# Kernel tuning notes

Hardware: AMD Instinct MI355X
Metric: run time of the kernel (lower is better)

## Reference

```python
import jax, jax.numpy as jnp
import numpy as np

B, I, HID, H, KS = 64, 1024, 2048, 8, 4
D = HID // H  # head_size = 256; also BlockDiagonal block size = (2*I)//H = 256
EPS = 1e-5


def setup_inputs() -> dict:
    key = jax.random.key(0)
    ks = jax.random.split(key, 16)
    r = lambda i, shape, s=0.02: jax.random.normal(ks[i], shape, dtype=jnp.float32) * s
    z = lambda shape: jnp.zeros(shape, jnp.float32)
    return {
        "x": jax.random.normal(ks[0], (B, I), dtype=jnp.float32),
        "h_prev": z((B, H, D)),
        "c_prev": z((B, H, D, D)),
        "n_prev": z((B, H, D)),
        "m_prev": z((B, H)),
        "ln_w": jnp.ones((I,), jnp.float32), "ln_b": z((I,)),
        "W_ul": r(1, (I, HID)), "b_ul": z((HID,)),
        "W_ur": r(2, (I, HID)), "b_ur": z((HID,)),
        "W_conv": r(3, (HID, HID, KS)), "b_conv": z((HID,)),
        "W_skip": r(4, (HID, HID)), "b_skip": z((HID,)),
        "W_q": r(5, (H, D, D)), "b_q": z((HID,)),
        "W_k": r(6, (H, D, D)), "b_k": z((HID,)),
        "W_v": r(7, (H, D, D)), "b_v": z((HID,)),
        "W_i": r(8, (HID, H)), "b_i": z((H,)),
        "W_f": r(9, (HID, H)), "b_f": z((H,)),
        "W_o": r(10, (HID, HID)), "b_o": z((HID,)),
        "W_down": r(11, (HID, I)), "b_down": z((I,)),
        "gn_w": jnp.ones((HID,), jnp.float32), "gn_b": z((HID,)),
    }


def _block_diag(zf, W, b):
    # BlockDiagonal: chunk last dim into H blocks, per-block Linear, concat -> [B,H,D]
    zh = zf.reshape(zf.shape[0], H, -1)
    return jnp.einsum('bhi,hio->bho', zh, W) + b.reshape(H, -1)


def reference(x, h_prev, c_prev, n_prev, m_prev, ln_w, ln_b, W_ul, b_ul, W_ur, b_ur,
              W_conv, b_conv, W_skip, b_skip, W_q, b_q, W_k, b_k, W_v, b_v,
              W_i, b_i, W_f, b_f, W_o, b_o, W_down, b_down, gn_w, gn_b):
    # LayerNorm
    mu = x.mean(-1, keepdims=True)
    var = jnp.mean((x - mu) ** 2, -1, keepdims=True)
    xn = (x - mu) * jax.lax.rsqrt(var + EPS) * ln_w + ln_b
    # Up projections
    xl = xn @ W_ul + b_ul            # [B, 2I] == [B, HID]
    xr = xn @ W_ur + b_ur
    # Causal conv over a length-1 sequence: after left padding + slicing, only the
    # last kernel tap (index KS-1) touches real data -> linear map with W_conv[:,:,KS-1]
    xc = jax.nn.silu(xl @ W_conv[:, :, KS - 1].T + b_conv)
    x_skip = xc @ W_skip + b_skip    # [B, HID]
    q = _block_diag(xc, W_q, b_q)                       # [B,H,D]
    k = _block_diag(xc, W_k, b_k) / jnp.sqrt(jnp.float32(D))
    v = _block_diag(xl, W_v, b_v)
    i_t = xc @ W_i + b_i             # [B,H]
    f_t = xc @ W_f + b_f
    o = jax.nn.sigmoid(xl @ W_o + b_o).reshape(-1, H, D)
    # Stabilized exponential gating
    m_t = jnp.maximum(f_t + m_prev, i_t)
    i_g = jnp.exp(i_t - m_t)
    f_g = jnp.exp(f_t + m_prev - m_t)
    # Outer-product state update + bilinear readout
    c_t = f_g[..., None, None] * c_prev + i_g[..., None, None] * jnp.einsum('bhd,bhk->bhdk', v, k)
    n_t = f_g[..., None] * n_prev + i_g[..., None] * k
    num = jnp.einsum('bhdk,bhk->bhd', c_t, q)
    den = jnp.clip(jnp.einsum('bhd,bhd->bh', n_t, q), 1.0, None)[..., None]
    h_t = o * num / den              # [B,H,D]
    # GroupNorm with num_groups == num_heads: normalize per head
    g_mu = h_t.mean(-1, keepdims=True)
    g_var = jnp.mean((h_t - g_mu) ** 2, -1, keepdims=True)
    gn = ((h_t - g_mu) * jax.lax.rsqrt(g_var + EPS)).reshape(-1, HID) * gn_w + gn_b
    out = (gn + x_skip) * jax.nn.silu(xr)
    out = out @ W_down + b_down
    final = out + x
    return (final, h_t, c_t, n_t, m_t)
```

## Files before the change

### kernel.cpp

```cpp
#include <hip/hip_runtime.h>
#include <cstddef>

typedef __bf16 bf16;
typedef __bf16 bf16x8 __attribute__((ext_vector_type(8)));
typedef short  s16x8  __attribute__((ext_vector_type(8)));
typedef float  f32x4  __attribute__((ext_vector_type(4)));

template <class T> T&& declv() noexcept;
template <class, class = void> struct takes_bf16vec { static constexpr bool value = false; };
template <class V> struct takes_bf16vec<V, decltype((void)__builtin_amdgcn_mfma_f32_16x16x32_bf16(
    declv<V>(), declv<V>(), declv<f32x4>(), 0, 0, 0))> { static constexpr bool value = true; };

template <class V>
__device__ __forceinline__ f32x4 mfma_bf16_16x16x32(V a, V b, f32x4 c) {
  if constexpr (takes_bf16vec<V>::value) {
    return __builtin_amdgcn_mfma_f32_16x16x32_bf16(a, b, c, 0, 0, 0);
  } else {
    return __builtin_amdgcn_mfma_f32_16x16x32_bf16(
        __builtin_bit_cast(s16x8, a), __builtin_bit_cast(s16x8, b), c, 0, 0, 0);
  }
}

constexpr int M_NONE = 0, M_SILU = 1, M_SIG = 2;

__global__ __launch_bounds__(256) void repack_wc(const float* __restrict__ Wc,
                                                 bf16* __restrict__ Wp) {
  const int n = blockIdx.x;
  const float4* src = (const float4*)(Wc + (size_t)n * 8192);
  bf16* dst = Wp + (size_t)n * 2048;
  for (int k = threadIdx.x; k < 2048; k += 256) {
    const float4 t = src[k];
    dst[k] = (bf16)t.w;
  }
}

__global__ __launch_bounds__(256) void ln_kernel(const float* __restrict__ x,
                                                 const float* __restrict__ w,
                                                 const float* __restrict__ bs,
                                                 const float* __restrict__ bdown,
                                                 bf16* __restrict__ xn,
                                                 float* __restrict__ outf) {
  const int b = blockIdx.x, tid = threadIdx.x;
  __shared__ float red[256];
  float vals[4];
  float s = 0.f;
#pragma unroll
  for (int i = 0; i < 4; ++i) { vals[i] = x[b * 1024 + i * 256 + tid]; s += vals[i]; }
  red[tid] = s; __syncthreads();
  for (int off = 128; off; off >>= 1) { if (tid < off) red[tid] += red[tid + off]; __syncthreads(); }
  const float mu = red[0] * (1.f / 1024.f);
  __syncthreads();
  float s2 = 0.f;
#pragma unroll
  for (int i = 0; i < 4; ++i) { const float d = vals[i] - mu; s2 += d * d; }
  red[tid] = s2; __syncthreads();
  for (int off = 128; off; off >>= 1) { if (tid < off) red[tid] += red[tid + off]; __syncthreads(); }
  const float rs = rsqrtf(red[0] * (1.f / 1024.f) + 1e-5f);
#pragma unroll
  for (int i = 0; i < 4; ++i) {
    const int j = i * 256 + tid;
    xn[b * 1024 + j] = (bf16)((vals[i] - mu) * rs * w[j] + bs[j]);
    outf[b * 1024 + j] = vals[i] + bdown[j];
  }
}

template <int K, int KS, int NTILES, bool BT, bool DUAL, bool ATOMIC>
__global__ __launch_bounds__(256) void gemm_part(
    const bf16* __restrict__ A0, const bf16* __restrict__ A1,
    const float* __restrict__ W0, const float* __restrict__ W1,
    const bf16* __restrict__ Wb,
    int ldA, int ldB, float* __restrict__ dst, int outN) {
  constexpr int Ncomb = NTILES * 16;
  constexpr int Kslice = K / KS;
  constexpr int chunk = Kslice / 4;
  const int tid = threadIdx.x;
  const int lane = tid & 63, wave = tid >> 6;
  const int l15 = lane & 15, quad = lane >> 4;
  const int tile = blockIdx.x % NTILES, ks = blockIdx.x / NTILES;

  const bf16* A = A0;
  const float* W = W0;
  int ncol;
  if (DUAL) {
    const int seg = tile >> 7;
    if (seg) { A = A1; W = W1; }
    ncol = (tile & 127) * 16;
  } else {
    ncol = tile * 16;
  }
  const int kbeg = ks * Kslice + wave * chunk;

  f32x4 acc0{}, acc1{}, acc2{}, acc3{};
#pragma unroll
  for (int k = 0; k < chunk; k += 32) {
    const int kk = kbeg + k + quad * 8;
    bf16x8 bfrag;
    if (BT) {
      bfrag = *(const bf16x8*)(Wb + (size_t)(ncol + l15) * K + kk);
    } else {
      const float* wp = W + (size_t)kk * ldB + ncol + l15;
#pragma unroll
      for (int j = 0; j < 8; ++j) bfrag[j] = (bf16)wp[(size_t)j * ldB];
    }
    const bf16* ap = A + (size_t)l15 * ldA + kk;
    const size_t st = (size_t)16 * ldA;
    bf16x8 a0 = *(const bf16x8*)(ap);
    bf16x8 a1 = *(const bf16x8*)(ap + st);
    bf16x8 a2 = *(const bf16x8*)(ap + 2 * st);
    bf16x8 a3 = *(const bf16x8*)(ap + 3 * st);
    acc0 = mfma_bf16_16x16x32(a0, bfrag, acc0);
    acc1 = mfma_bf16_16x16x32(a1, bfrag, acc1);
    acc2 = mfma_bf16_16x16x32(a2, bfrag, acc2);
    acc3 = mfma_bf16_16x16x32(a3, bfrag, acc3);
  }
  __shared__ float lds[4][64][20];
#pragma unroll
  for (int r = 0; r < 4; ++r) {
    const int rr = quad * 4 + r;
    lds[wave][rr][l15]      = acc0[r];
    lds[wave][16 + rr][l15] = acc1[r];
    lds[wave][32 + rr][l15] = acc2[r];
    lds[wave][48 + rr][l15] = acc3[r];
  }
  __syncthreads();
  const int col = tid & 15, rb = (tid >> 4) << 2;
#pragma unroll
  for (int r2 = 0; r2 < 4; ++r2) {
    const int row = rb + r2;
    const float v = lds[0][row][col] + lds[1][row][col] + lds[2][row][col] + lds[3][row][col];
    if (ATOMIC) {
      atomicAdd(dst + (size_t)row * outN + tile * 16 + col, v);
    } else {
      dst[((size_t)ks * 64 + row) * Ncomb + tile * 16 + col] = v;
    }
  }
}

__global__ __launch_bounds__(256) void combine(
    const float* __restrict__ part, int KS, int Ncomb, int halfN,
    const float* __restrict__ bias0, const float* __restrict__ bias1,
    int mode0, int mode1,
    float* __restrict__ outF0, bf16* __restrict__ outB0,
    float* __restrict__ outF1, bf16* __restrict__ outB1) {
  const int e = (blockIdx.x * 256 + threadIdx.x) * 4;
  const int total = 64 * Ncomb;
  if (e >= total) return;
  const int row = e / Ncomb, col = e - row * Ncomb;
  float4 s = *(const float4*)(part + e);
  for (int ks = 1; ks < KS; ++ks) {
    const float4 p = *(const float4*)(part + (size_t)ks * total + e);
    s.x += p.x; s.y += p.y; s.z += p.z; s.w += p.w;
  }
  const int seg = (col >= halfN) ? 1 : 0;
  const int cn = col - seg * halfN;
  const float* bias = seg ? bias1 : bias0;
  const int mode = seg ? mode1 : mode0;
  float* outF = seg ? outF1 : outF0;
  bf16* outB = seg ? outB1 : outB0;
  float vv[4] = {s.x, s.y, s.z, s.w};
#pragma unroll
  for (int j = 0; j < 4; ++j) {
    float v = vv[j] + bias[cn + j];
    if (mode == M_SILU)       v = v / (1.f + expf(-v));
    else if (mode == M_SIG)   v = 1.f / (1.f + expf(-v));
    const size_t oi = (size_t)row * halfN + cn + j;
    if (outF) outF[oi] = v;
    if (outB) outB[oi] = (bf16)v;
  }
}

__global__ __launch_bounds__(256) void gemm_qkv(
    const bf16* __restrict__ xc, const bf16* __restrict__ xl,
    const float* __restrict__ Wq, const float* __restrict__ bq,
    const float* __restrict__ Wk, const float* __restrict__ bk,
    const float* __restrict__ Wv, const float* __restrict__ bv,
    float* __restrict__ qf, float* __restrict__ kf, float* __restrict__ vf) {
  const int tid = threadIdx.x;
  const int lane = tid & 63, wave = tid >> 6;
  const int l15 = lane & 15, quad = lane >> 4;
  const int seg = blockIdx.x >> 7, t = blockIdx.x & 127;
  const int n0 = t * 16, h = t >> 4, wn0 = n0 & 255;
  const bf16* A = (seg == 2) ? xl : xc;
  const float* W = (seg == 0) ? Wq : (seg == 1) ? Wk : Wv;
  const float* bias = (seg == 0) ? bq : (seg == 1) ? bk : bv;
  float* out = (seg == 0) ? qf : (seg == 1) ? kf : vf;
  const float* Wb = W + (size_t)h * 65536;
  const int aCol0 = h << 8;
  const int kbeg = wave * 64;

  f32x4 acc0{}, acc1{}, acc2{}, acc3{};
#pragma unroll
  for (int k = 0; k < 64; k += 32) {
    const int kk = kbeg + k + quad * 8;
    bf16x8 bfrag;
    const float* wp = Wb + (size_t)kk * 256 + wn0 + l15;
#pragma unroll
    for (int j = 0; j < 8; ++j) bfrag[j] = (bf16)wp[(size_t)j * 256];
    const bf16* ap = A + (size_t)l15 * 2048 + aCol0 + kk;
    const size_t st = (size_t)16 * 2048;
    bf16x8 a0 = *(const bf16x8*)(ap);
    bf16x8 a1 = *(const bf16x8*)(ap + st);
    bf16x8 a2 = *(const bf16x8*)(ap + 2 * st);
    bf16x8 a3 = *(const bf16x8*)(ap + 3 * st);
    acc0 = mfma_bf16_16x16x32(a0, bfrag, acc0);
    acc1 = mfma_bf16_16x16x32(a1, bfrag, acc1);
    acc2 = mfma_bf16_16x16x32(a2, bfrag, acc2);
    acc3 = mfma_bf16_16x16x32(a3, bfrag, acc3);
  }
  __shared__ float lds[4][64][20];
#pragma unroll
  for (int r = 0; r < 4; ++r) {
    const int rr = quad * 4 + r;
    lds[wave][rr][l15]      = acc0[r];
    lds[wave][16 + rr][l15] = acc1[r];
    lds[wave][32 + rr][l15] = acc2[r];
    lds[wave][48 + rr][l15] = acc3[r];
  }
  __syncthreads();
  const int col = tid & 15, rb = (tid >> 4) << 2;
  const float bv_ = bias[n0 + col];
#pragma unroll
  for (int r2 = 0; r2 < 4; ++r2) {
    const int row = rb + r2;
    float v = lds[0][row][col] + lds[1][row][col] + lds[2][row][col] + lds[3][row][col] + bv_;
    if (seg == 1) v *= 0.0625f;
    out[(size_t)row * 2048 + n0 + col] = v;
  }
}

__global__ __launch_bounds__(256) void gates_kernel(
    const bf16* __restrict__ xc, const float* __restrict__ Wi, const float* __restrict__ bi,
    const float* __restrict__ Wf, const float* __restrict__ bfv, const float* __restrict__ m_prev,
    float* __restrict__ ig, float* __restrict__ fg, float* __restrict__ mt_out) {
  const int b = blockIdx.x, tid = threadIdx.x;
  float ai[8] = {}, af[8] = {};
  for (int k = tid; k < 2048; k += 256) {
    const float xv = (float)xc[b * 2048 + k];
    const float4 wi0 = *(const float4*)(Wi + (size_t)k * 8);
    const float4 wi1 = *(const float4*)(Wi + (size_t)k * 8 + 4);
    const float4 wf0 = *(const float4*)(Wf + (size_t)k * 8);
    const float4 wf1 = *(const float4*)(Wf + (size_t)k * 8 + 4);
    ai[0] += xv * wi0.x; ai[1] += xv * wi0.y; ai[2] += xv * wi0.z; ai[3] += xv * wi0.w;
    ai[4] += xv * wi1.x; ai[5] += xv * wi1.y; ai[6] += xv * wi1.z; ai[7] += xv * wi1.w;
    af[0] += xv * wf0.x; af[1] += xv * wf0.y; af[2] += xv * wf0.z; af[3] += xv * wf0.w;
    af[4] += xv * wf1.x; af[5] += xv * wf1.y; af[6] += xv * wf1.z; af[7] += xv * wf1.w;
  }
  __shared__ float ri[256][8], rf[256][8];
#pragma unroll
  for (int h = 0; h < 8; ++h) { ri[tid][h] = ai[h]; rf[tid][h] = af[h]; }
  __syncthreads();
  for (int off = 128; off; off >>= 1) {
    if (tid < off) {
#pragma unroll
      for (int h = 0; h < 8; ++h) { ri[tid][h] += ri[tid + off][h]; rf[tid][h] += rf[tid + off][h]; }
    }
    __syncthreads();
  }
  if (tid < 8) {
    const float it = ri[0][tid] + bi[tid];
    const float ft = rf[0][tid] + bfv[tid];
    const float mp = m_prev[b * 8 + tid];
    const float mt = fmaxf(ft + mp, it);
    mt_out[b * 8 + tid] = mt;
    ig[b * 8 + tid] = expf(it - mt);
    fg[b * 8 + tid] = expf(ft + mp - mt);
  }
}

__global__ __launch_bounds__(256) void state1(
    const float* __restrict__ c_prev, const float* __restrict__ qf,
    const float* __restrict__ kf, const float* __restrict__ vf,
    const float* __restrict__ ig, const float* __restrict__ fg,
    float* __restrict__ ct_out, float* __restrict__ numw) {
  const int bh = blockIdx.x >> 3, rg = blockIdx.x & 7;
  const int tid = threadIdx.x;
  const int b = bh >> 3, h = bh & 7, vb = b * 2048 + h * 256;
  __shared__ float q_s[256], k_s[256];
  q_s[tid] = qf[vb + tid];
  k_s[tid] = kf[vb + tid];
  __syncthreads();
  const float i_g = ig[bh], f_g = fg[bh];
  const int row = rg * 32 + (tid >> 3);
  const int lane8 = tid & 7;
  const float vd = vf[vb + row];
  const float iv = i_g * vd;
  const size_t base = ((size_t)bh << 16) + ((size_t)row << 8) + lane8 * 4;
  float p = 0.f;
#pragma unroll
  for (int i = 0; i < 8; ++i) {
    const int c = lane8 * 4 + i * 32;
    const float4 cp = *(const float4*)(c_prev + base + i * 32);
    float4 cn;
    cn.x = f_g * cp.x + iv * k_s[c];
    cn.y = f_g * cp.y + iv * k_s[c + 1];
    cn.z = f_g * cp.z + iv * k_s[c + 2];
    cn.w = f_g * cp.w + iv * k_s[c + 3];
    *(float4*)(ct_out + base + i * 32) = cn;
    p += cn.x * q_s[c] + cn.y * q_s[c + 1] + cn.z * q_s[c + 2] + cn.w * q_s[c + 3];
  }
#pragma unroll
  for (int m = 1; m < 8; m <<= 1) p += __shfl_xor(p, m, 64);
  if (lane8 == 0) numw[bh * 256 + row] = p;
}

__global__ __launch_bounds__(256) void state2(
    const float* __restrict__ n_prev, const float* __restrict__ qf,
    const float* __restrict__ kf, const float* __restrict__ of,
    const float* __restrict__ ig, const float* __restrict__ fg,
    const float* numw, const float* __restrict__ xskip,
    const float* __restrict__ xrf, const float* __restrict__ gnw,
    const float* __restrict__ gnb, float* __restrict__ nt_out,
    float* ht_out, bf16* __restrict__ pre_bf) {
  const int bh = blockIdx.x, b = bh >> 3, h = bh & 7;
  const int tid = threadIdx.x;
  const int vb = b * 2048 + h * 256;
  __shared__ float red[256];
  const float i_g = ig[bh], f_g = fg[bh];
  const float qv = qf[vb + tid], kv = kf[vb + tid];
  const float nv = f_g * n_prev[bh * 256 + tid] + i_g * kv;
  nt_out[bh * 256 + tid] = nv;
  red[tid] = nv * qv;
  __syncthreads();
  for (int off = 128; off; off >>= 1) { if (tid < off) red[tid] += red[tid + off]; __syncthreads(); }
  const float den = fmaxf(red[0], 1.0f);
  const float num = numw[bh * 256 + tid];
  const float hv = of[vb + tid] * num / den;
  ht_out[bh * 256 + tid] = hv;
  __syncthreads();
  red[tid] = hv; __syncthreads();
  for (int off = 128; off; off >>= 1) { if (tid < off) red[tid] += red[tid + off]; __syncthreads(); }
  const float mu = red[0] * (1.f / 256.f);
  __syncthreads();
  const float dv = hv - mu;
  red[tid] = dv * dv; __syncthreads();
  for (int off = 128; off; off >>= 1) { if (tid < off) red[tid] += red[tid + off]; __syncthreads(); }
  const float gn = (hv - mu) * rsqrtf(red[0] * (1.f / 256.f) + 1e-5f);
  const int j = h * 256 + tid;
  const float xr = xrf[b * 2048 + j];
  const float pre = (gn * gnw[j] + gnb[j] + xskip[b * 2048 + j]) * (xr / (1.f + expf(-xr)));
  pre_bf[b * 2048 + j] = (bf16)pre;
}

extern "C" void kernel_launch(void* const* d_in, const int* in_sizes, int n_in,
                              void* d_out, int out_size, void* d_ws, size_t ws_size,
                              hipStream_t stream) {
  (void)in_sizes; (void)n_in; (void)out_size; (void)ws_size;
  const float* x      = (const float*)d_in[0];
  const float* c_prev = (const float*)d_in[2];
  const float* n_prev = (const float*)d_in[3];
  const float* m_prev = (const float*)d_in[4];
  const float* ln_w = (const float*)d_in[5];
  const float* ln_b = (const float*)d_in[6];
  const float* W_ul = (const float*)d_in[7];
  const float* b_ul = (const float*)d_in[8];
  const float* W_ur = (const float*)d_in[9];
  const float* b_ur = (const float*)d_in[10];
  const float* W_conv = (const float*)d_in[11];
  const float* b_conv = (const float*)d_in[12];
  const float* W_skip = (const float*)d_in[13];
  const float* b_skip = (const float*)d_in[14];
  const float* W_q = (const float*)d_in[15];
  const float* b_q = (const float*)d_in[16];
  const float* W_k = (const float*)d_in[17];
  const float* b_k = (const float*)d_in[18];
  const float* W_v = (const float*)d_in[19];
  const float* b_v = (const float*)d_in[20];
  const float* W_i = (const float*)d_in[21];
  const float* b_i = (const float*)d_in[22];
  const float* W_f = (const float*)d_in[23];
  const float* b_f = (const float*)d_in[24];
  const float* W_o = (const float*)d_in[25];
  const float* b_o = (const float*)d_in[26];
  const float* W_down = (const float*)d_in[27];
  const float* b_down = (const float*)d_in[28];
  const float* gn_w = (const float*)d_in[29];
  const float* gn_b = (const float*)d_in[30];

  float* out_final = (float*)d_out;
  float* out_ht = out_final + 65536;
  float* out_ct = out_final + 196608;
  float* out_nt = out_final + 33751040;
  float* out_mt = out_final + 33882112;

  char* ws = (char*)d_ws;
  bf16*  xn_bf   = (bf16*)(ws + 0);
  bf16*  xl_bf   = (bf16*)(ws + 131072);
  bf16*  xc_bf   = (bf16*)(ws + 393216);
  bf16*  pre_bf  = (bf16*)(ws + 655360);
  float* xr_f    = (float*)(ws + 917504);
  float* xskip_f = (float*)(ws + 1441792);
  float* q_f     = (float*)(ws + 1966080);
  float* k_f     = (float*)(ws + 2490368);
  float* v_f     = (float*)(ws + 3014656);
  float* o_f     = (float*)(ws + 3538944);
  float* ig_f    = (float*)(ws + 4063232);
  float* fg_f    = (float*)(ws + 4065280);
  bf16*  wcp     = (bf16*)(ws + 4067328);
  float* num_f   = out_ht;
  float* part    = out_ct;

  repack_wc<<<2048, 256, 0, stream>>>(W_conv, wcp);
  ln_kernel<<<64, 256, 0, stream>>>(x, ln_w, ln_b, b_down, xn_bf, out_final);
  gemm_part<1024, 4, 256, false, true, false><<<1024, 256, 0, stream>>>(
      xn_bf, xn_bf, W_ul, W_ur, nullptr, 1024, 2048, part, 0);
  combine<<<256, 256, 0, stream>>>(part, 4, 4096, 2048, b_ul, b_ur, M_NONE, M_NONE,
                                   nullptr, xl_bf, xr_f, nullptr);
  gemm_part<2048, 8, 128, true, false, false><<<1024, 256, 0, stream>>>(
      xl_bf, nullptr, nullptr, nullptr, wcp, 2048, 2048, part, 0);
  combine<<<128, 256, 0, stream>>>(part, 8, 2048, 2048, b_conv, nullptr, M_SILU, M_NONE,
                                   nullptr, xc_bf, nullptr, nullptr);
  gemm_part<2048, 4, 256, false, true, false><<<1024, 256, 0, stream>>>(
      xc_bf, xl_bf, W_skip, W_o, nullptr, 2048, 2048, part, 0);
  combine<<<256, 256, 0, stream>>>(part, 4, 4096, 2048, b_skip, b_o, M_NONE, M_SIG,
                                   xskip_f, nullptr, o_f, nullptr);
  gemm_qkv<<<384, 256, 0, stream>>>(xc_bf, xl_bf, W_q, b_q, W_k, b_k, W_v, b_v,
                                    q_f, k_f, v_f);
  gates_kernel<<<64, 256, 0, stream>>>(xc_bf, W_i, b_i, W_f, b_f, m_prev, ig_f, fg_f, out_mt);
  state1<<<4096, 256, 0, stream>>>(c_prev, q_f, k_f, v_f, ig_f, fg_f, out_ct, num_f);
  state2<<<512, 256, 0, stream>>>(n_prev, q_f, k_f, o_f, ig_f, fg_f, num_f,
                                  xskip_f, xr_f, gn_w, gn_b, out_nt, out_ht, pre_bf);
  gemm_part<2048, 8, 64, false, false, true><<<512, 256, 0, stream>>>(
      pre_bf, nullptr, W_down, nullptr, nullptr, 2048, 1024, out_final, 1024);
}
```

Before: 440.3 us.

## Fuse GEMM stages, drop split-K combine passes and conv weight repack

Replaces the split-K GEMMs plus separate combine kernels with full-K tile kernels that apply bias and activation in their epilogue. The conv weight tap is now read straight from W_conv with a strided access instead of going through a repack kernel. The skip/o, qkv and gate computations are merged into one launch, and the two state kernels are merged into one. This cuts launches and partial-sum traffic, but each GEMM now launches far fewer blocks (128–256), so the GPU may be underused and the conv weight loads are strided.

New measurement: 424.9 us, median of 2. 1.04x faster.

```diff
diff --git a/kernel.cpp b/kernel.cpp
--- a/kernel.cpp
+++ b/kernel.cpp
@@ -22,17 +22,6 @@
 }
 
 constexpr int M_NONE = 0, M_SILU = 1, M_SIG = 2;
-
-__global__ __launch_bounds__(256) void repack_wc(const float* __restrict__ Wc,
-                                                 bf16* __restrict__ Wp) {
-  const int n = blockIdx.x;
-  const float4* src = (const float4*)(Wc + (size_t)n * 8192);
-  bf16* dst = Wp + (size_t)n * 2048;
-  for (int k = threadIdx.x; k < 2048; k += 256) {
-    const float4 t = src[k];
-    dst[k] = (bf16)t.w;
-  }
-}
 
 __global__ __launch_bounds__(256) void ln_kernel(const float* __restrict__ x,
                                                  const float* __restrict__ w,
@@ -64,30 +53,244 @@
   }
 }
 
-template <int K, int KS, int NTILES, bool BT, bool DUAL, bool ATOMIC>
-__global__ __launch_bounds__(256) void gemm_part(
+template <int K, bool TAP>
+__device__ __forceinline__ void gemm_tile(
+    const bf16* __restrict__ A, int ldA, int aOff,
+    const float* __restrict__ W, int ldB, int wcol,
+    const float* __restrict__ bias, int bOff, float scale, int mode,
+    float* __restrict__ outF, bf16* __restrict__ outB, int outLd, int oOff,
+    float lds[4][64][20]) {
+  const int tid = threadIdx.x;
+  const int lane = tid & 63, wave = tid >> 6;
+  const int l15 = lane & 15, quad = lane >> 4;
+  constexpr int chunk = K / 4;
+  const int kbeg = wave * chunk;
+  f32x4 acc0{}, acc1{}, acc2{}, acc3{};
+#pragma unroll 4
+  for (int k = 0; k < chunk; k += 32) {
+    const int kk = kbeg + k + quad * 8;
+    bf16x8 bfrag;
+    if (TAP) {
+      const float* wp = W + ((size_t)(wcol + l15) * K + kk) * 4 + 3;
+#pragma unroll
+      for (int j = 0; j < 8; ++j) bfrag[j] = (bf16)wp[j * 4];
+    } else {
+      const float* wp = W + (size_t)kk * ldB + wcol + l15;
+#pragma unroll
+      for (int j = 0; j < 8; ++j) bfrag[j] = (bf16)wp[(size_t)j * ldB];
+    }
+    const bf16* ap = A + (size_t)l15 * ldA + aOff + kk;
+    const size_t st = (size_t)16 * ldA;
+    bf16x8 a0 = *(const bf16x8*)(ap);
+    bf16x8 a1 = *(const bf16x8*)(ap + st);
+    bf16x8 a2 = *(const bf16x8*)(ap + 2 * st);
+    bf16x8 a3 = *(const bf16x8*)(ap + 3 * st);
+    acc0 = mfma_bf16_16x16x32(a0, bfrag, acc0);
+    acc1 = mfma_bf16_16x16x32(a1, bfrag, acc1);
+    acc2 = mfma_bf16_16x16x32(a2, bfrag, acc2);
+    acc3 = mfma_bf16_16x16x32(a3, bfrag, acc3);
+  }
+#pragma unroll
+  for (int r = 0; r < 4; ++r) {
+    const int rr = quad * 4 + r;
+    lds[wave][rr][l15]      = acc0[r];
+    lds[wave][16 + rr][l15] = acc1[r];
+    lds[wave][32 + rr][l15] = acc2[r];
+    lds[wave][48 + rr][l15] = acc3[r];
+  }
+  __syncthreads();
+  const int col = tid & 15, rb = (tid >> 4) << 2;
+  const float bvv = bias[bOff + col];
+#pragma unroll
+  for (int r2 = 0; r2 < 4; ++r2) {
+    const int row = rb + r2;
+    float v = (lds[0][row][col] + lds[1][row][col] + lds[2][row][col] + lds[3][row][col] + bvv) * scale;
+    if (mode == M_SILU)      v = v / (1.f + expf(-v));
+    else if (mode == M_SIG)  v = 1.f / (1.f + expf(-v));
+    const size_t oi = (size_t)row * outLd + oOff + col;
+    if (outF) outF[oi] = v;
+    if (outB) outB[oi] = (bf16)v;
+  }
+}
+
+template <int K, bool TAP, bool DUAL>
+__global__ __launch_bounds__(256) void gemm_full(
     const bf16* __restrict__ A0, const bf16* __restrict__ A1,
     const float* __restrict__ W0, const float* __restrict__ W1,
-    const bf16* __restrict__ Wb,
+    int ldA, int ldB,
+    const float* __restrict__ bias0, const float* __restrict__ bias1,
+    int mode0, int mode1,
+    float* __restrict__ outF0, bf16* __restrict__ outB0,
+    float* __restrict__ outF1, bf16* __restrict__ outB1, int outLd) {
+  __shared__ float lds[4][64][20];
+  const int tile = blockIdx.x;
+  if (DUAL) {
+    const int ncol = (tile & 127) * 16;
+    if (tile >> 7) {
+      gemm_tile<K, TAP>(A1, ldA, 0, W1, ldB, ncol, bias1, ncol, 1.f, mode1,
+                        outF1, outB1, outLd, ncol, lds);
+    } else {
+      gemm_tile<K, TAP>(A0, ldA, 0, W0, ldB, ncol, bias0, ncol, 1.f, mode0,
+                        outF0, outB0, outLd, ncol, lds);
+    }
+  } else {
+    const int ncol = tile * 16;
+    gemm_tile<K, TAP>(A0, ldA, 0, W0, ldB, ncol, bias0, ncol, 1.f, mode0,
+                      outF0, outB0, outLd, ncol, lds);
+  }
+}
+
+__global__ __launch_bounds__(256) void mega_c(
+    const bf16* __restrict__ xc, const bf16* __restrict__ xl,
+    const float* __restrict__ W_skip, const float* __restrict__ b_skip,
+    const float* __restrict__ W_o, const float* __restrict__ b_o,
+    const float* __restrict__ Wq, const float* __restrict__ bq,
+    const float* __restrict__ Wk, const float* __restrict__ bk,
+    const float* __restrict__ Wv, const float* __restrict__ bv,
+    const float* __restrict__ Wi, const float* __restrict__ bi,
+    const float* __restrict__ Wf, const float* __restrict__ bfv,
+    const float* __restrict__ m_prev,
+    float* __restrict__ xskip_f, float* __restrict__ o_f,
+    float* __restrict__ qf, float* __restrict__ kf, float* __restrict__ vf,
+    float* __restrict__ ig, float* __restrict__ fgo, float* __restrict__ mt_out) {
+  __shared__ float lds[4][64][20];
+  const int bid = blockIdx.x;
+  if (bid < 256) {
+    const int seg = bid >> 7, ncol = (bid & 127) * 16;
+    if (seg) {
+      gemm_tile<2048, false>(xl, 2048, 0, W_o, 2048, ncol, b_o, ncol, 1.f, M_SIG,
+                             o_f, nullptr, 2048, ncol, lds);
+    } else {
+      gemm_tile<2048, false>(xc, 2048, 0, W_skip, 2048, ncol, b_skip, ncol, 1.f, M_NONE,
+                             xskip_f, nullptr, 2048, ncol, lds);
+    }
+  } else if (bid < 640) {
+    const int t6 = bid - 256;
+    const int seg = t6 >> 7, t = t6 & 127;
+    const int n0 = t * 16, h = t >> 4;
+    const bf16* A = (seg == 2) ? xl : xc;
+    const float* W = (seg == 0) ? Wq : (seg == 1) ? Wk : Wv;
+    const float* bias = (seg == 0) ? bq : (seg == 1) ? bk : bv;
+    float* out = (seg == 0) ? qf : (seg == 1) ? kf : vf;
+    gemm_tile<256, false>(A, 2048, h << 8, W + (size_t)h * 65536, 256, n0 & 255,
+                          bias, n0, (seg == 1) ? 0.0625f : 1.f, M_NONE,
+                          out, nullptr, 2048, n0, lds);
+  } else {
+    const int b = bid - 640, tid = threadIdx.x;
+    float* shf = &lds[0][0][0];
+    float (*ri)[8] = reinterpret_cast<float(*)[8]>(shf);
+    float (*rf)[8] = reinterpret_cast<float(*)[8]>(shf + 2048);
+    float ai[8] = {}, af[8] = {};
+    for (int k = tid; k < 2048; k += 256) {
+      const float xv = (float)xc[b * 2048 + k];
+      const float4 wi0 = *(const float4*)(Wi + (size_t)k * 8);
+      const float4 wi1 = *(const float4*)(Wi + (size_t)k * 8 + 4);
+      const float4 wf0 = *(const float4*)(Wf + (size_t)k * 8);
+      const float4 wf1 = *(const float4*)(Wf + (size_t)k * 8 + 4);
+      ai[0] += xv * wi0.x; ai[1] += xv * wi0.y; ai[2] += xv * wi0.z; ai[3] += xv * wi0.w;
+      ai[4] += xv * wi1.x; ai[5] += xv * wi1.y; ai[6] += xv * wi1.z; ai[7] += xv * wi1.w;
+      af[0] += xv * wf0.x; af[1] += xv * wf0.y; af[2] += xv * wf0.z; af[3] += xv * wf0.w;
+      af[4] += xv * wf1.x; af[5] += xv * wf1.y; af[6] += xv * wf1.z; af[7] += xv * wf1.w;
+    }
+#pragma unroll
+    for (int h = 0; h < 8; ++h) { ri[tid][h] = ai[h]; rf[tid][h] = af[h]; }
+    __syncthreads();
+    for (int off = 128; off; off >>= 1) {
+      if (tid < off) {
+#pragma unroll
+        for (int h = 0; h < 8; ++h) { ri[tid][h] += ri[tid + off][h]; rf[tid][h] += rf[tid + off][h]; }
+      }
+      __syncthreads();
+    }
+    if (tid < 8) {
+      const float it = ri[0][tid] + bi[tid];
+      const float ft = rf[0][tid] + bfv[tid];
+      const float mp = m_prev[b * 8 + tid];
+      const float mt = fmaxf(ft + mp, it);
+      mt_out[b * 8 + tid] = mt;
+      ig[b * 8 + tid] = expf(it - mt);
+      fgo[b * 8 + tid] = expf(ft + mp - mt);
+    }
+  }
+}
+
+__global__ __launch_bounds__(256) void state_fused(
+    const float* __restrict__ c_prev, const float* __restrict__ n_prev,
+    const float* __restrict__ qf, const float* __restrict__ kf,
+    const float* __restrict__ vf, const float* __restrict__ of,
+    const float* __restrict__ ig, const float* __restrict__ fg,
+    const float* __restrict__ xskip, const float* __restrict__ xrf,
+    const float* __restrict__ gnw, const float* __restrict__ gnb,
+    float* __restrict__ ct_out, float* __restrict__ nt_out,
+    float* __restrict__ ht_out, bf16* __restrict__ pre_bf) {
+  const int bh = blockIdx.x, b = bh >> 3, h = bh & 7;
+  const int tid = threadIdx.x;
+  const int vb = b * 2048 + h * 256;
+  __shared__ float q_s[256], k_s[256], num_s[256], red[256];
+  q_s[tid] = qf[vb + tid];
+  k_s[tid] = kf[vb + tid];
+  const float i_g = ig[bh], f_g = fg[bh];
+  __syncthreads();
+  const int lane8 = tid & 7, rowbase = tid >> 3;
+#pragma unroll
+  for (int rg = 0; rg < 8; ++rg) {
+    const int row = rg * 32 + rowbase;
+    const float iv = i_g * vf[vb + row];
+    const size_t base = ((size_t)bh << 16) + ((size_t)row << 8) + lane8 * 4;
+    float p = 0.f;
+#pragma unroll
+    for (int i = 0; i < 8; ++i) {
+      const int c = lane8 * 4 + i * 32;
+      const float4 cp = *(const float4*)(c_prev + base + i * 32);
+      float4 cn;
+      cn.x = f_g * cp.x + iv * k_s[c];
+      cn.y = f_g * cp.y + iv * k_s[c + 1];
+      cn.z = f_g * cp.z + iv * k_s[c + 2];
+      cn.w = f_g * cp.w + iv * k_s[c + 3];
+      *(float4*)(ct_out + base + i * 32) = cn;
+      p += cn.x * q_s[c] + cn.y * q_s[c + 1] + cn.z * q_s[c + 2] + cn.w * q_s[c + 3];
+    }
+    p += __shfl_xor(p, 1, 64);
+    p += __shfl_xor(p, 2, 64);
+    p += __shfl_xor(p, 4, 64);
+    if (lane8 == 0) num_s[row] = p;
+  }
+  __syncthreads();
+  const float qv = q_s[tid], kv = k_s[tid];
+  const float nv = f_g * n_prev[bh * 256 + tid] + i_g * kv;
+  nt_out[bh * 256 + tid] = nv;
+  red[tid] = nv * qv;
+  __syncthreads();
+  for (int off = 128; off; off >>= 1) { if (tid < off) red[tid] += red[tid + off]; __syncthreads(); }
+  const float den = fmaxf(red[0], 1.0f);
+  const float hv = of[vb + tid] * num_s[tid] / den;
+  ht_out[bh * 256 + tid] = hv;
+  __syncthreads();
+  red[tid] = hv; __syncthreads();
+  for (int off = 128; off; off >>= 1) { if (tid < off) red[tid] += red[tid + off]; __syncthreads(); }
+  const float mu = red[0] * (1.f / 256.f);
+  __syncthreads();
+  const float dv = hv - mu;
+  red[tid] = dv * dv; __syncthreads();
+  for (int off = 128; off; off >>= 1) { if (tid < off) red[tid] += red[tid + off]; __syncthreads(); }
+  const float gn = (hv - mu) * rsqrtf(red[0] * (1.f / 256.f) + 1e-5f);
+  const int j = h * 256 + tid;
+  const float xr = xrf[b * 2048 + j];
+  const float pre = (gn * gnw[j] + gnb[j] + xskip[b * 2048 + j]) * (xr / (1.f + expf(-xr)));
+  pre_bf[b * 2048 + j] = (bf16)pre;
+}
+
+template <int K, int KS, int NTILES>
+__global__ __launch_bounds__(256) void gemm_atomic(
+    const bf16* __restrict__ A, const float* __restrict__ W,
     int ldA, int ldB, float* __restrict__ dst, int outN) {
-  constexpr int Ncomb = NTILES * 16;
   constexpr int Kslice = K / KS;
   constexpr int chunk = Kslice / 4;
   const int tid = threadIdx.x;
   const int lane = tid & 63, wave = tid >> 6;
   const int l15 = lane & 15, quad = lane >> 4;
   const int tile = blockIdx.x % NTILES, ks = blockIdx.x / NTILES;
-
-  const bf16* A = A0;
-  const float* W = W0;
-  int ncol;
-  if (DUAL) {
-    const int seg = tile >> 7;
-    if (seg) { A = A1; W = W1; }
-    ncol = (tile & 127) * 16;
-  } else {
-    ncol = tile * 16;
-  }
+  const int ncol = tile * 16;
   const int kbeg = ks * Kslice + wave * chunk;
 
   f32x4 acc0{}, acc1{}, acc2{}, acc3{};
@@ -95,13 +298,9 @@
   for (int k = 0; k < chunk; k += 32) {
     const int kk = kbeg + k + quad * 8;
     bf16x8 bfrag;
-    if (BT) {
-      bfrag = *(const bf16x8*)(Wb + (size_t)(ncol + l15) * K + kk);
-    } else {
-      const float* wp = W + (size_t)kk * ldB + ncol + l15;
-#pragma unroll
-      for (int j = 0; j < 8; ++j) bfrag[j] = (bf16)wp[(size_t)j * ldB];
-    }
+    const float* wp = W + (size_t)kk * ldB + ncol + l15;
+#pragma unroll
+    for (int j = 0; j < 8; ++j) bfrag[j] = (bf16)wp[(size_t)j * ldB];
     const bf16* ap = A + (size_t)l15 * ldA + kk;
     const size_t st = (size_t)16 * ldA;
     bf16x8 a0 = *(const bf16x8*)(ap);
@@ -128,217 +327,8 @@
   for (int r2 = 0; r2 < 4; ++r2) {
     const int row = rb + r2;
     const float v = lds[0][row][col] + lds[1][row][col] + lds[2][row][col] + lds[3][row][col];
-    if (ATOMIC) {
-      atomicAdd(dst + (size_t)row * outN + tile * 16 + col, v);
-    } else {
-      dst[((size_t)ks * 64 + row) * Ncomb + tile * 16 + col] = v;
-    }
-  }
-}
-
-__global__ __launch_bounds__(256) void combine(
-    const float* __restrict__ part, int KS, int Ncomb, int halfN,
-    const float* __restrict__ bias0, const float* __restrict__ bias1,
-    int mode0, int mode1,
-    float* __restrict__ outF0, bf16* __restrict__ outB0,
-    float* __restrict__ outF1, bf16* __restrict__ outB1) {
-  const int e = (blockIdx.x * 256 + threadIdx.x) * 4;
-  const int total = 64 * Ncomb;
-  if (e >= total) return;
-  const int row = e / Ncomb, col = e - row * Ncomb;
-  float4 s = *(const float4*)(part + e);
-  for (int ks = 1; ks < KS; ++ks) {
-    const float4 p = *(const float4*)(part + (size_t)ks * total + e);
-    s.x += p.x; s.y += p.y; s.z += p.z; s.w += p.w;
-  }
-  const int seg = (col >= halfN) ? 1 : 0;
-  const int cn = col - seg * halfN;
-  const float* bias = seg ? bias1 : bias0;
-  const int mode = seg ? mode1 : mode0;
-  float* outF = seg ? outF1 : outF0;
-  bf16* outB = seg ? outB1 : outB0;
-  float vv[4] = {s.x, s.y, s.z, s.w};
-#pragma unroll
-  for (int j = 0; j < 4; ++j) {
-    float v = vv[j] + bias[cn + j];
-    if (mode == M_SILU)       v = v / (1.f + expf(-v));
-    else if (mode == M_SIG)   v = 1.f / (1.f + expf(-v));
-    const size_t oi = (size_t)row * halfN + cn + j;
-    if (outF) outF[oi] = v;
-    if (outB) outB[oi] = (bf16)v;
-  }
-}
-
-__global__ __launch_bounds__(256) void gemm_qkv(
-    const bf16* __restrict__ xc, const bf16* __restrict__ xl,
-    const float* __restrict__ Wq, const float* __restrict__ bq,
-    const float* __restrict__ Wk, const float* __restrict__ bk,
-    const float* __restrict__ Wv, const float* __restrict__ bv,
-    float* __restrict__ qf, float* __restrict__ kf, float* __restrict__ vf) {
-  const int tid = threadIdx.x;
-  const int lane = tid & 63, wave = tid >> 6;
-  const int l15 = lane & 15, quad = lane >> 4;
-  const int seg = blockIdx.x >> 7, t = blockIdx.x & 127;
-  const int n0 = t * 16, h = t >> 4, wn0 = n0 & 255;
-  const bf16* A = (seg == 2) ? xl : xc;
-  const float* W = (seg == 0) ? Wq : (seg == 1) ? Wk : Wv;
-  const float* bias = (seg == 0) ? bq : (seg == 1) ? bk : bv;
-  float* out = (seg == 0) ? qf : (seg == 1) ? kf : vf;
-  const float* Wb = W + (size_t)h * 65536;
-  const int aCol0 = h << 8;
-  const int kbeg = wave * 64;
-
-  f32x4 acc0{}, acc1{}, acc2{}, acc3{};
-#pragma unroll
-  for (int k = 0; k < 64; k += 32) {
-    const int kk = kbeg + k + quad * 8;
-    bf16x8 bfrag;
-    const float* wp = Wb + (size_t)kk * 256 + wn0 + l15;
-#pragma unroll
-    for (int j = 0; j < 8; ++j) bfrag[j] = (bf16)wp[(size_t)j * 256];
-    const bf16* ap = A + (size_t)l15 * 2048 + aCol0 + kk;
-    const size_t st = (size_t)16 * 2048;
-    bf16x8 a0 = *(const bf16x8*)(ap);
-    bf16x8 a1 = *(const bf16x8*)(ap + st);
-    bf16x8 a2 = *(const bf16x8*)(ap + 2 * st);
-    bf16x8 a3 = *(const bf16x8*)(ap + 3 * st);
-    acc0 = mfma_bf16_16x16x32(a0, bfrag, acc0);
-    acc1 = mfma_bf16_16x16x32(a1, bfrag, acc1);
-    acc2 = mfma_bf16_16x16x32(a2, bfrag, acc2);
-    acc3 = mfma_bf16_16x16x32(a3, bfrag, acc3);
-  }
-  __shared__ float lds[4][64][20];
-#pragma unroll
-  for (int r = 0; r < 4; ++r) {
-    const int rr = quad * 4 + r;
-    lds[wave][rr][l15]      = acc0[r];
-    lds[wave][16 + rr][l15] = acc1[r];
-    lds[wave][32 + rr][l15] = acc2[r];
-    lds[wave][48 + rr][l15] = acc3[r];
-  }
-  __syncthreads();
-  const int col = tid & 15, rb = (tid >> 4) << 2;
-  const float bv_ = bias[n0 + col];
-#pragma unroll
-  for (int r2 = 0; r2 < 4; ++r2) {
-    const int row = rb + r2;
-    float v = lds[0][row][col] + lds[1][row][col] + lds[2][row][col] + lds[3][row][col] + bv_;
-    if (seg == 1) v *= 0.0625f;
-    out[(size_t)row * 2048 + n0 + col] = v;
-  }
-}
-
-__global__ __launch_bounds__(256) void gates_kernel(
-    const bf16* __restrict__ xc, const float* __restrict__ Wi, const float* __restrict__ bi,
-    const float* __restrict__ Wf, const float* __restrict__ bfv, const float* __restrict__ m_prev,
-    float* __restrict__ ig, float* __restrict__ fg, float* __restrict__ mt_out) {
-  const int b = blockIdx.x, tid = threadIdx.x;
-  float ai[8] = {}, af[8] = {};
-  for (int k = tid; k < 2048; k += 256) {
-    const float xv = (float)xc[b * 2048 + k];
-    const float4 wi0 = *(const float4*)(Wi + (size_t)k * 8);
-    const float4 wi1 = *(const float4*)(Wi + (size_t)k * 8 + 4);
-    const float4 wf0 = *(const float4*)(Wf + (size_t)k * 8);
-    const float4 wf1 = *(const float4*)(Wf + (size_t)k * 8 + 4);
-    ai[0] += xv * wi0.x; ai[1] += xv * wi0.y; ai[2] += xv * wi0.z; ai[3] += xv * wi0.w;
-    ai[4] += xv * wi1.x; ai[5] += xv * wi1.y; ai[6] += xv * wi1.z; ai[7] += xv * wi1.w;
-    af[0] += xv * wf0.x; af[1] += xv * wf0.y; af[2] += xv * wf0.z; af[3] += xv * wf0.w;
-    af[4] += xv * wf1.x; af[5] += xv * wf1.y; af[6] += xv * wf1.z; af[7] += xv * wf1.w;
-  }
-  __shared__ float ri[256][8], rf[256][8];
-#pragma unroll
-  for (int h = 0; h < 8; ++h) { ri[tid][h] = ai[h]; rf[tid][h] = af[h]; }
-  __syncthreads();
-  for (int off = 128; off; off >>= 1) {
-    if (tid < off) {
-#pragma unroll
-      for (int h = 0; h < 8; ++h) { ri[tid][h] += ri[tid + off][h]; rf[tid][h] += rf[tid + off][h]; }
-    }
-    __syncthreads();
-  }
-  if (tid < 8) {
-    const float it = ri[0][tid] + bi[tid];
-    const float ft = rf[0][tid] + bfv[tid];
-    const float mp = m_prev[b * 8 + tid];
-    const float mt = fmaxf(ft + mp, it);
-    mt_out[b * 8 + tid] = mt;
-    ig[b * 8 + tid] = expf(it - mt);
-    fg[b * 8 + tid] = expf(ft + mp - mt);
-  }
-}
-
-__global__ __launch_bounds__(256) void state1(
-    const float* __restrict__ c_prev, const float* __restrict__ qf,
-    const float* __restrict__ kf, const float* __restrict__ vf,
-    const float* __restrict__ ig, const float* __restrict__ fg,
-    float* __restrict__ ct_out, float* __restrict__ numw) {
-  const int bh = blockIdx.x >> 3, rg = blockIdx.x & 7;
-  const int tid = threadIdx.x;
-  const int b = bh >> 3, h = bh & 7, vb = b * 2048 + h * 256;
-  __shared__ float q_s[256], k_s[256];
-  q_s[tid] = qf[vb + tid];
-  k_s[tid] = kf[vb + tid];
-  __syncthreads();
-  const float i_g = ig[bh], f_g = fg[bh];
-  const int row = rg * 32 + (tid >> 3);
-  const int lane8 = tid & 7;
-  const float vd = vf[vb + row];
-  const float iv = i_g * vd;
-  const size_t base = ((size_t)bh << 16) + ((size_t)row << 8) + lane8 * 4;
-  float p = 0.f;
-#pragma unroll
-  for (int i = 0; i < 8; ++i) {
-    const int c = lane8 * 4 + i * 32;
-    const float4 cp = *(const float4*)(c_prev + base + i * 32);
-    float4 cn;
-    cn.x = f_g * cp.x + iv * k_s[c];
-    cn.y = f_g * cp.y + iv * k_s[c + 1];
-    cn.z = f_g * cp.z + iv * k_s[c + 2];
-    cn.w = f_g * cp.w + iv * k_s[c + 3];
-    *(float4*)(ct_out + base + i * 32) = cn;
-    p += cn.x * q_s[c] + cn.y * q_s[c + 1] + cn.z * q_s[c + 2] + cn.w * q_s[c + 3];
-  }
-#pragma unroll
-  for (int m = 1; m < 8; m <<= 1) p += __shfl_xor(p, m, 64);
-  if (lane8 == 0) numw[bh * 256 + row] = p;
-}
-
-__global__ __launch_bounds__(256) void state2(
-    const float* __restrict__ n_prev, const float* __restrict__ qf,
-    const float* __restrict__ kf, const float* __restrict__ of,
-    const float* __restrict__ ig, const float* __restrict__ fg,
-    const float* numw, const float* __restrict__ xskip,
-    const float* __restrict__ xrf, const float* __restrict__ gnw,
-    const float* __restrict__ gnb, float* __restrict__ nt_out,
-    float* ht_out, bf16* __restrict__ pre_bf) {
-  const int bh = blockIdx.x, b = bh >> 3, h = bh & 7;
-  const int tid = threadIdx.x;
-  const int vb = b * 2048 + h * 256;
-  __shared__ float red[256];
-  const float i_g = ig[bh], f_g = fg[bh];
-  const float qv = qf[vb + tid], kv = kf[vb + tid];
-  const float nv = f_g * n_prev[bh * 256 + tid] + i_g * kv;
-  nt_out[bh * 256 + tid] = nv;
-  red[tid] = nv * qv;
-  __syncthreads();
-  for (int off = 128; off; off >>= 1) { if (tid < off) red[tid] += red[tid + off]; __syncthreads(); }
-  const float den = fmaxf(red[0], 1.0f);
-  const float num = numw[bh * 256 + tid];
-  const float hv = of[vb + tid] * num / den;
-  ht_out[bh * 256 + tid] = hv;
-  __syncthreads();
-  red[tid] = hv; __syncthreads();
-  for (int off = 128; off; off >>= 1) { if (tid < off) red[tid] += red[tid + off]; __syncthreads(); }
-  const float mu = red[0] * (1.f / 256.f);
-  __syncthreads();
-  const float dv = hv - mu;
-  red[tid] = dv * dv; __syncthreads();
-  for (int off = 128; off; off >>= 1) { if (tid < off) red[tid] += red[tid + off]; __syncthreads(); }
-  const float gn = (hv - mu) * rsqrtf(red[0] * (1.f / 256.f) + 1e-5f);
-  const int j = h * 256 + tid;
-  const float xr = xrf[b * 2048 + j];
-  const float pre = (gn * gnw[j] + gnb[j] + xskip[b * 2048 + j]) * (xr / (1.f + expf(-xr)));
-  pre_bf[b * 2048 + j] = (bf16)pre;
+    atomicAdd(dst + (size_t)row * outN + ncol + col, v);
+  }
 }
 
 extern "C" void kernel_launch(void* const* d_in, const int* in_sizes, int n_in,
@@ -395,30 +385,20 @@
   float* o_f     = (float*)(ws + 3538944);
   float* ig_f    = (float*)(ws + 4063232);
   float* fg_f    = (float*)(ws + 4065280);
-  bf16*  wcp     = (bf16*)(ws + 4067328);
-  float* num_f   = out_ht;
-  float* part    = out_ct;
-
-  repack_wc<<<2048, 256, 0, stream>>>(W_conv, wcp);
+
   ln_kernel<<<64, 256, 0, stream>>>(x, ln_w, ln_b, b_down, xn_bf, out_final);
-  gemm_part<1024, 4, 256, false, true, false><<<1024, 256, 0, stream>>>(
-      xn_bf, xn_bf, W_ul, W_ur, nullptr, 1024, 2048, part, 0);
-  combine<<<256, 256, 0, stream>>>(part, 4, 4096, 2048, b_ul, b_ur, M_NONE, M_NONE,
-                                   nullptr, xl_bf, xr_f, nullptr);
-  gemm_part<2048, 8, 128, true, false, false><<<1024, 256, 0, stream>>>(
-      xl_bf, nullptr, nullptr, nullptr, wcp, 2048, 2048, part, 0);
-  combine<<<128, 256, 0, stream>>>(part, 8, 2048, 2048, b_conv, nullptr, M_SILU, M_NONE,
-                                   nullptr, xc_bf, nullptr, nullptr);
-  gemm_part<2048, 4, 256, false, true, false><<<1024, 256, 0, stream>>>(
-      xc_bf, xl_bf, W_skip, W_o, nullptr, 2048, 2048, part, 0);
-  combine<<<256, 256, 0, stream>>>(part, 4, 4096, 2048, b_skip, b_o, M_NONE, M_SIG,
-                                   xskip_f, nullptr, o_f, nullptr);
-  gemm_qkv<<<384, 256, 0, stream>>>(xc_bf, xl_bf, W_q, b_q, W_k, b_k, W_v, b_v,
-                                    q_f, k_f, v_f);
-  gates_kernel<<<64, 256, 0, stream>>>(xc_bf, W_i, b_i, W_f, b_f, m_prev, ig_f, fg_f, out_mt);
-  state1<<<4096, 256, 0, stream>>>(c_prev, q_f, k_f, v_f, ig_f, fg_f, out_ct, num_f);
-  state2<<<512, 256, 0, stream>>>(n_prev, q_f, k_f, o_f, ig_f, fg_f, num_f,
-                                  xskip_f, xr_f, gn_w, gn_b, out_nt, out_ht, pre_bf);
-  gemm_part<2048, 8, 64, false, false, true><<<512, 256, 0, stream>>>(
-      pre_bf, nullptr, W_down, nullptr, nullptr, 2048, 1024, out_final, 1024);
-}
+  gemm_full<1024, false, true><<<256, 256, 0, stream>>>(
+      xn_bf, xn_bf, W_ul, W_ur, 1024, 2048,
+      b_ul, b_ur, M_NONE, M_NONE, nullptr, xl_bf, xr_f, nullptr, 2048);
+  gemm_full<2048, true, false><<<128, 256, 0, stream>>>(
+      xl_bf, nullptr, W_conv, nullptr, 2048, 0,
+      b_conv, nullptr, M_SILU, M_NONE, nullptr, xc_bf, nullptr, nullptr, 2048);
+  mega_c<<<704, 256, 0, stream>>>(
+      xc_bf, xl_bf, W_skip, b_skip, W_o, b_o, W_q, b_q, W_k, b_k, W_v, b_v,
+      W_i, b_i, W_f, b_f, m_prev, xskip_f, o_f, q_f, k_f, v_f, ig_f, fg_f, out_mt);
+  state_fused<<<512, 256, 0, stream>>>(
+      c_prev, n_prev, q_f, k_f, v_f, o_f, ig_f, fg_f,
+      xskip_f, xr_f, gn_w, gn_b, out_ct, out_nt, out_ht, pre_bf);
+  gemm_atomic<2048, 8, 64><<<512, 256, 0, stream>>>(
+      pre_bf, W_down, 2048, 1024, out_final, 1024);
+}
```
